# Optimization experiments

Measured on AMD Instinct MI355X. Metric: run time of the kernel, lower is better.

The kernel has to match this reference:

```python
import jax, jax.numpy as jnp
import numpy as np


def setup_inputs() -> dict:
    key = jax.random.key(0)
    ks = jax.random.split(key, 7)
    C = 256
    Cqk = C // 8  # 32
    B, D, H, W = 4, 16, 16, 16
    s_in = 1.0 / np.sqrt(C)  # conv1x1 fan_in = C
    return {
        "x": jax.random.normal(ks[0], (B, C, D, H, W), dtype=jnp.float32),
        "Wq": jax.random.uniform(ks[1], (Cqk, C), jnp.float32, -s_in, s_in),
        "bq": jax.random.uniform(ks[2], (Cqk,), jnp.float32, -s_in, s_in),
        "Wk": jax.random.uniform(ks[3], (Cqk, C), jnp.float32, -s_in, s_in),
        "bk": jax.random.uniform(ks[4], (Cqk,), jnp.float32, -s_in, s_in),
        "Wv": jax.random.uniform(ks[5], (C, C), jnp.float32, -s_in, s_in),
        "bv": jax.random.uniform(ks[6], (C,), jnp.float32, -s_in, s_in),
    }


def reference(x, Wq, bq, Wk, bk, Wv, bv):
    B, C, D, H, W = x.shape
    N = D * H * W
    xf = x.reshape(B, C, N)  # [B, C, N]
    # 1x1x1 convs == per-voxel GEMMs over the channel dim
    q = jnp.einsum('oc,bcn->bon', Wq, xf) + bq[None, :, None]  # [B, Cqk, N]
    k = jnp.einsum('oc,bcn->bon', Wk, xf) + bk[None, :, None]  # [B, Cqk, N]
    v = jnp.einsum('oc,bcn->bon', Wv, xf) + bv[None, :, None]  # [B, C, N]
    # attention[b, n, m] = softmax_m( q[:, n] . k[:, m] )
    scores = jnp.einsum('bcn,bcm->bnm', q, k)  # [B, N, N]
    attn = jax.nn.softmax(scores, axis=-1)
    # out = value @ attention^T  -> out[b, c, n] = sum_m v[b,c,m] * attn[b,n,m]
    out = jnp.einsum('bcm,bnm->bcn', v, attn)
    return x + out.reshape(B, C, D, H, W)
```

## Files before the change

kernel.cpp:

```cpp
#include <hip/hip_runtime.h>
#include <math.h>

#define B_   4
#define C_   256
#define CQK  32
#define N_   4096
#define TQ   32
#define TM   64

typedef __attribute__((ext_vector_type(8))) short short8;
typedef __attribute__((ext_vector_type(4))) short short4v;
typedef __attribute__((ext_vector_type(4))) float f32x4;
typedef __attribute__((ext_vector_type(2))) unsigned int uint2v;

__device__ __forceinline__ unsigned short f2bf(float f) {
    unsigned u = __builtin_bit_cast(unsigned, f);
    u += 0x7fffu + ((u >> 16) & 1u);
    return (unsigned short)(u >> 16);
}

__global__ __launch_bounds__(256) void cvt_w(
    const float* __restrict__ Wq, const float* __restrict__ bq,
    const float* __restrict__ Wk, const float* __restrict__ bk,
    const float* __restrict__ Wv, const float* __restrict__ bv,
    unsigned short* __restrict__ wbf, float* __restrict__ biasf)
{
    const int r = blockIdx.x;
    const int t = threadIdx.x;
    const float* src = (r < 32) ? (Wq + r * C_)
                     : (r < 64) ? (Wk + (r - 32) * C_)
                                : (Wv + (r - 64) * C_);
    wbf[r * C_ + t] = f2bf(src[t]);
    if (t == 0)
        biasf[r] = (r < 32) ? bq[r] : (r < 64) ? bk[r - 32] : bv[r - 64];
}

__global__ __launch_bounds__(256) void proj_qkv(
    const float* __restrict__ x, const unsigned short* __restrict__ wbf,
    const float* __restrict__ biasf,
    unsigned short* __restrict__ qb, unsigned short* __restrict__ kb,
    unsigned short* __restrict__ vb)
{
    __shared__ __align__(16) unsigned short xs[64 * 136];

    const int t    = threadIdx.x;
    const int w    = t >> 6;
    const int lane = t & 63;
    const int quad = lane >> 4;
    const int c16  = lane & 15;
    const int n0   = blockIdx.x * 64;
    const int b    = blockIdx.y;

    f32x4 acc[5][4];
#pragma unroll
    for (int i = 0; i < 5; ++i)
#pragma unroll
        for (int nt = 0; nt < 4; ++nt) acc[i][nt] = (f32x4){0.f, 0.f, 0.f, 0.f};

#pragma unroll
    for (int half = 0; half < 2; ++half) {
        __syncthreads();
#pragma unroll
        for (int pass = 0; pass < 8; ++pass) {
            const int c  = 128 * half + pass * 16 + (t >> 4);
            const int nq = (t & 15) * 4;
            const f32x4 xv = *(const f32x4*)&x[((size_t)(b * C_) + c) * N_ + n0 + nq];
            const int cl = c - 128 * half;
            xs[(nq + 0) * 136 + cl] = f2bf(xv.x);
            xs[(nq + 1) * 136 + cl] = f2bf(xv.y);
            xs[(nq + 2) * 136 + cl] = f2bf(xv.z);
            xs[(nq + 3) * 136 + cl] = f2bf(xv.w);
        }
        __syncthreads();
#pragma unroll
        for (int ks = 0; ks < 4; ++ks) {
            short8 af[5], bf[4];
#pragma unroll
            for (int i = 0; i < 5; ++i) {
                const int o = (5 * w + i) * 16 + c16;
                af[i] = *(const short8*)&wbf[o * C_ + half * 128 + ks * 32 + quad * 8];
            }
#pragma unroll
            for (int nt = 0; nt < 4; ++nt)
                bf[nt] = *(const short8*)&xs[(16 * nt + c16) * 136 + ks * 32 + quad * 8];
#pragma unroll
            for (int i = 0; i < 5; ++i)
#pragma unroll
                for (int nt = 0; nt < 4; ++nt)
                    acc[i][nt] = __builtin_amdgcn_mfma_f32_16x16x32_bf16(af[i], bf[nt], acc[i][nt], 0, 0, 0);
        }
    }

#pragma unroll
    for (int i = 0; i < 5; ++i) {
        const int OT = 5 * w + i;
        const int obase = OT * 16 + 4 * quad;
        const f32x4 bv4 = *(const f32x4*)&biasf[obase];
#pragma unroll
        for (int nt = 0; nt < 4; ++nt) {
            const int n = n0 + 16 * nt + c16;
            float vals[4];
#pragma unroll
            for (int r = 0; r < 4; ++r) vals[r] = acc[i][nt][r] + bv4[r];
            if (OT < 4) {
                unsigned short* dst = (OT < 2) ? qb : kb;
                const int o = obase - ((OT < 2) ? 0 : 32);
                short4v pk;
#pragma unroll
                for (int r = 0; r < 4; ++r) pk[r] = (short)f2bf(vals[r]);
                *(short4v*)&dst[((size_t)(b * N_) + n) * 32 + o] = pk;
            } else {
#pragma unroll
                for (int r = 0; r < 4; ++r) {
                    const int c = obase + r - 64;
                    vb[((size_t)(b * C_) + c) * N_ + n] = f2bf(vals[r]);
                }
            }
        }
    }
}

__global__ __launch_bounds__(256) void attn_kernel(
    const float* __restrict__ x,
    const unsigned short* __restrict__ qg,
    const unsigned short* __restrict__ kg,
    const unsigned short* __restrict__ vg,
    float* __restrict__ out)
{
    __shared__ __align__(16) unsigned short qs[TQ * 40];
    __shared__ __align__(16) unsigned short ks[TM * 40];
    __shared__ __align__(16) unsigned short vs[256 * 64];
    __shared__ __align__(16) unsigned short ps[TQ * 72];
    __shared__ float ls[2 * TQ];

    const int t    = threadIdx.x;
    const int w    = t >> 6;
    const int lane = t & 63;
    const int quad = lane >> 4;
    const int c16  = lane & 15;
    const int b    = blockIdx.y;
    const int q0   = blockIdx.x * TQ;
    const int qh   = w & 1;
    const int kh   = w >> 1;

    if (t < 128) {
        const int row = t >> 2, seg = t & 3;
        *(short8*)&qs[row * 40 + seg * 8] =
            *(const short8*)(qg + ((size_t)(b * N_) + q0 + row) * 32 + seg * 8);
    }

    short8 kpre, vpre[8];
    {
        const int row = t >> 2, seg = t & 3;
        kpre = *(const short8*)(kg + ((size_t)(b * N_) + row) * 32 + seg * 8);
        const int vc = t >> 3, vch = t & 7;
#pragma unroll
        for (int p = 0; p < 8; ++p)
            vpre[p] = *(const short8*)(vg + ((size_t)(b * C_) + vc + 32 * p) * N_ + vch * 8);
    }

    f32x4 O[4][2];
#pragma unroll
    for (int ct = 0; ct < 4; ++ct)
#pragma unroll
        for (int qt = 0; qt < 2; ++qt) O[ct][qt] = (f32x4){0.f, 0.f, 0.f, 0.f};

    float l_run = 0.0f;

#pragma unroll 1
    for (int it = 0; it < N_ / TM; ++it) {
        __syncthreads();
        {
            const int row = t >> 2, seg = t & 3;
            *(short8*)&ks[row * 40 + seg * 8] = kpre;
            const int vc0 = t >> 3, vch = t & 7;
#pragma unroll
            for (int p = 0; p < 8; ++p) {
                const int c = vc0 + 32 * p;
                *(short8*)&vs[c * 64 + 8 * (vch ^ (c & 7))] = vpre[p];
            }
        }
        __syncthreads();
        if (it < N_ / TM - 1) {
            const int m1 = (it + 1) * TM;
            const int row = t >> 2, seg = t & 3;
            kpre = *(const short8*)(kg + ((size_t)(b * N_) + m1 + row) * 32 + seg * 8);
            const int vc = t >> 3, vch = t & 7;
#pragma unroll
            for (int p = 0; p < 8; ++p)
                vpre[p] = *(const short8*)(vg + ((size_t)(b * C_) + vc + 32 * p) * N_ + m1 + vch * 8);
        }

        const short8 bqf = *(const short8*)&qs[(16 * qh + c16) * 40 + quad * 8];
        float rs = 0.f;
#pragma unroll
        for (int f = 0; f < 2; ++f) {
            const short8 akf = *(const short8*)&ks[(32 * kh + 16 * f + c16) * 40 + quad * 8];
            const f32x4 z = {0.f, 0.f, 0.f, 0.f};
            const f32x4 sf = __builtin_amdgcn_mfma_f32_16x16x32_bf16(akf, bqf, z, 0, 0, 0);
            float p4[4];
#pragma unroll
            for (int r = 0; r < 4; ++r) { p4[r] = __expf(sf[r]); rs += p4[r]; }
            uint2v u;
            u.x = (unsigned)f2bf(p4[0]) | ((unsigned)f2bf(p4[1]) << 16);
            u.y = (unsigned)f2bf(p4[2]) | ((unsigned)f2bf(p4[3]) << 16);
            *(uint2v*)&ps[(16 * qh + c16) * 72 + 32 * kh + 16 * f + 4 * quad] = u;
        }
        rs += __shfl_xor(rs, 16);
        rs += __shfl_xor(rs, 32);
        l_run += rs;
        __syncthreads();

#pragma unroll
        for (int s = 0; s < 2; ++s) {
            const short8 bp0 = *(const short8*)&ps[(c16) * 72 + 32 * s + 8 * quad];
            const short8 bp1 = *(const short8*)&ps[(16 + c16) * 72 + 32 * s + 8 * quad];
#pragma unroll
            for (int ct = 0; ct < 4; ++ct) {
                const int c = 64 * w + 16 * ct + c16;
                const short8 av = *(const short8*)&vs[c * 64 + 8 * ((4 * s + quad) ^ (c & 7))];
                O[ct][0] = __builtin_amdgcn_mfma_f32_16x16x32_bf16(av, bp0, O[ct][0], 0, 0, 0);
                O[ct][1] = __builtin_amdgcn_mfma_f32_16x16x32_bf16(av, bp1, O[ct][1], 0, 0, 0);
            }
        }
    }

    if (quad == 0) ls[kh * TQ + 16 * qh + c16] = l_run;
    __syncthreads();

#pragma unroll
    for (int qt = 0; qt < 2; ++qt) {
        const int q = 16 * qt + c16;
        const float li = 1.0f / (ls[q] + ls[TQ + q]);
        const int n = q0 + q;
#pragma unroll
        for (int ct = 0; ct < 4; ++ct) {
#pragma unroll
            for (int r = 0; r < 4; ++r) {
                const int c = 64 * w + 16 * ct + 4 * quad + r;
                const size_t idx = ((size_t)(b * C_) + c) * N_ + n;
                out[idx] = x[idx] + O[ct][qt][r] * li;
            }
        }
    }
}

extern "C" void kernel_launch(void* const* d_in, const int* in_sizes, int n_in,
                              void* d_out, int out_size, void* d_ws, size_t ws_size,
                              hipStream_t stream) {
    const float* x  = (const float*)d_in[0];
    const float* Wq = (const float*)d_in[1];
    const float* bq = (const float*)d_in[2];
    const float* Wk = (const float*)d_in[3];
    const float* bk = (const float*)d_in[4];
    const float* Wv = (const float*)d_in[5];
    const float* bv = (const float*)d_in[6];
    float* out = (float*)d_out;

    unsigned short* ws16 = (unsigned short*)d_ws;
    unsigned short* qb  = ws16;
    unsigned short* kb  = qb + (size_t)B_ * N_ * 32;
    unsigned short* vb  = kb + (size_t)B_ * N_ * 32;
    unsigned short* wbf = vb + (size_t)B_ * C_ * N_;
    float* biasf = (float*)(wbf + 320 * C_);

    cvt_w<<<dim3(320), 256, 0, stream>>>(Wq, bq, Wk, bk, Wv, bv, wbf, biasf);
    proj_qkv<<<dim3(N_ / 64, B_), 256, 0, stream>>>(x, wbf, biasf, qb, kb, vb);
    attn_kernel<<<dim3(N_ / TQ, B_), 256, 0, stream>>>(x, qb, kb, vb, out);
}
```

Baseline: 176.9 us.

## Add bf16 transpose pass, drop LDS staging of K/V, widen attention tile

A new kernel transposes x into a bf16 [N,C] buffer so the projection kernel reads MFMA operands straight from global memory without LDS staging, using smaller 32-voxel tiles. The attention kernel moves to 512 threads and 64 queries per block. It reads K and V fragments directly from global/L2 instead of staging them in shared memory, and double-buffers the P tile so each iteration needs one barrier instead of three. The trade-offs are an extra global pass over x and heavier reliance on cache for V reuse, since V is re-read per wave rather than shared through LDS.

Result: slower. 244.6 us (+38.3%).

```diff
diff --git a/kernel.cpp b/kernel.cpp
--- a/kernel.cpp
+++ b/kernel.cpp
@@ -5,8 +5,10 @@
 #define C_   256
 #define CQK  32
 #define N_   4096
-#define TQ   32
+#define TQ   64
 #define TM   64
+#define ITERS (N_ / TM)
+#define PSS  72
 
 typedef __attribute__((ext_vector_type(8))) short short8;
 typedef __attribute__((ext_vector_type(4))) short short4v;
@@ -35,60 +37,65 @@
         biasf[r] = (r < 32) ? bq[r] : (r < 64) ? bk[r - 32] : bv[r - 64];
 }
 
+__global__ __launch_bounds__(256) void xpose(
+    const float* __restrict__ x, unsigned short* __restrict__ xT)
+{
+    const int n0 = blockIdx.x * 64;
+    const int b  = blockIdx.y;
+    const int nl = threadIdx.x & 63;
+    const int co = (threadIdx.x >> 6) * 8;
+
+    const float* xb = x + (size_t)(b * C_) * N_ + n0 + nl;
+    unsigned short* ob = xT + ((size_t)(b * N_) + n0 + nl) * C_;
+
+#pragma unroll
+    for (int pass = 0; pass < 8; ++pass) {
+        const int c0 = pass * 32 + co;
+        short8 pk;
+#pragma unroll
+        for (int j = 0; j < 8; ++j)
+            pk[j] = (short)f2bf(xb[(size_t)(c0 + j) * N_]);
+        *(short8*)(ob + c0) = pk;
+    }
+}
+
 __global__ __launch_bounds__(256) void proj_qkv(
-    const float* __restrict__ x, const unsigned short* __restrict__ wbf,
+    const unsigned short* __restrict__ xT, const unsigned short* __restrict__ wbf,
     const float* __restrict__ biasf,
     unsigned short* __restrict__ qb, unsigned short* __restrict__ kb,
     unsigned short* __restrict__ vb)
 {
-    __shared__ __align__(16) unsigned short xs[64 * 136];
-
     const int t    = threadIdx.x;
     const int w    = t >> 6;
     const int lane = t & 63;
     const int quad = lane >> 4;
     const int c16  = lane & 15;
-    const int n0   = blockIdx.x * 64;
+    const int n0   = blockIdx.x * 32;
     const int b    = blockIdx.y;
 
-    f32x4 acc[5][4];
+    f32x4 acc[5][2];
 #pragma unroll
     for (int i = 0; i < 5; ++i)
 #pragma unroll
-        for (int nt = 0; nt < 4; ++nt) acc[i][nt] = (f32x4){0.f, 0.f, 0.f, 0.f};
-
-#pragma unroll
-    for (int half = 0; half < 2; ++half) {
-        __syncthreads();
-#pragma unroll
-        for (int pass = 0; pass < 8; ++pass) {
-            const int c  = 128 * half + pass * 16 + (t >> 4);
-            const int nq = (t & 15) * 4;
-            const f32x4 xv = *(const f32x4*)&x[((size_t)(b * C_) + c) * N_ + n0 + nq];
-            const int cl = c - 128 * half;
-            xs[(nq + 0) * 136 + cl] = f2bf(xv.x);
-            xs[(nq + 1) * 136 + cl] = f2bf(xv.y);
-            xs[(nq + 2) * 136 + cl] = f2bf(xv.z);
-            xs[(nq + 3) * 136 + cl] = f2bf(xv.w);
-        }
-        __syncthreads();
-#pragma unroll
-        for (int ks = 0; ks < 4; ++ks) {
-            short8 af[5], bf[4];
-#pragma unroll
-            for (int i = 0; i < 5; ++i) {
-                const int o = (5 * w + i) * 16 + c16;
-                af[i] = *(const short8*)&wbf[o * C_ + half * 128 + ks * 32 + quad * 8];
-            }
-#pragma unroll
-            for (int nt = 0; nt < 4; ++nt)
-                bf[nt] = *(const short8*)&xs[(16 * nt + c16) * 136 + ks * 32 + quad * 8];
-#pragma unroll
-            for (int i = 0; i < 5; ++i)
-#pragma unroll
-                for (int nt = 0; nt < 4; ++nt)
-                    acc[i][nt] = __builtin_amdgcn_mfma_f32_16x16x32_bf16(af[i], bf[nt], acc[i][nt], 0, 0, 0);
-        }
+        for (int nt = 0; nt < 2; ++nt) acc[i][nt] = (f32x4){0.f, 0.f, 0.f, 0.f};
+
+    const unsigned short* xrow0 = xT + ((size_t)(b * N_) + n0 + c16) * C_ + quad * 8;
+    const unsigned short* wrow0 = wbf + (size_t)(80 * w + c16) * C_ + quad * 8;
+
+#pragma unroll
+    for (int ks = 0; ks < 8; ++ks) {
+        short8 af[5], bf[2];
+#pragma unroll
+        for (int i = 0; i < 5; ++i)
+            af[i] = *(const short8*)(wrow0 + (size_t)(16 * i) * C_ + 32 * ks);
+#pragma unroll
+        for (int nt = 0; nt < 2; ++nt)
+            bf[nt] = *(const short8*)(xrow0 + (size_t)(16 * nt) * C_ + 32 * ks);
+#pragma unroll
+        for (int i = 0; i < 5; ++i)
+#pragma unroll
+            for (int nt = 0; nt < 2; ++nt)
+                acc[i][nt] = __builtin_amdgcn_mfma_f32_16x16x32_bf16(af[i], bf[nt], acc[i][nt], 0, 0, 0);
     }
 
 #pragma unroll
@@ -97,7 +104,7 @@
         const int obase = OT * 16 + 4 * quad;
         const f32x4 bv4 = *(const f32x4*)&biasf[obase];
 #pragma unroll
-        for (int nt = 0; nt < 4; ++nt) {
+        for (int nt = 0; nt < 2; ++nt) {
             const int n = n0 + 16 * nt + c16;
             float vals[4];
 #pragma unroll
@@ -120,18 +127,15 @@
     }
 }
 
-__global__ __launch_bounds__(256) void attn_kernel(
+__global__ __launch_bounds__(512) void attn_kernel(
     const float* __restrict__ x,
     const unsigned short* __restrict__ qg,
     const unsigned short* __restrict__ kg,
     const unsigned short* __restrict__ vg,
     float* __restrict__ out)
 {
-    __shared__ __align__(16) unsigned short qs[TQ * 40];
-    __shared__ __align__(16) unsigned short ks[TM * 40];
-    __shared__ __align__(16) unsigned short vs[256 * 64];
-    __shared__ __align__(16) unsigned short ps[TQ * 72];
-    __shared__ float ls[2 * TQ];
+    __shared__ __align__(16) unsigned short ps[2][TQ * PSS];
+    __shared__ float ls[4 * TQ];
 
     const int t    = threadIdx.x;
     const int w    = t >> 6;
@@ -140,24 +144,15 @@
     const int c16  = lane & 15;
     const int b    = blockIdx.y;
     const int q0   = blockIdx.x * TQ;
-    const int qh   = w & 1;
-    const int kh   = w >> 1;
-
-    if (t < 128) {
-        const int row = t >> 2, seg = t & 3;
-        *(short8*)&qs[row * 40 + seg * 8] =
-            *(const short8*)(qg + ((size_t)(b * N_) + q0 + row) * 32 + seg * 8);
-    }
-
-    short8 kpre, vpre[8];
-    {
-        const int row = t >> 2, seg = t & 3;
-        kpre = *(const short8*)(kg + ((size_t)(b * N_) + row) * 32 + seg * 8);
-        const int vc = t >> 3, vch = t & 7;
-#pragma unroll
-        for (int p = 0; p < 8; ++p)
-            vpre[p] = *(const short8*)(vg + ((size_t)(b * C_) + vc + 32 * p) * N_ + vch * 8);
-    }
+    const int fs = w & 3, gp = w >> 2;
+    const int cg = w & 3, qh = w >> 2;
+
+    const unsigned short* kbase = kg + (size_t)(b * N_) * 32;
+    const unsigned short* vbase = vg + (size_t)(b * C_) * N_;
+
+    short8 bq0 = *(const short8*)(qg + ((size_t)(b * N_) + q0 + 16 * (2 * gp) + c16) * 32 + quad * 8);
+    short8 bq1 = *(const short8*)(qg + ((size_t)(b * N_) + q0 + 16 * (2 * gp + 1) + c16) * 32 + quad * 8);
+    short8 ak = *(const short8*)(kbase + (size_t)(fs * 16 + c16) * 32 + quad * 8);
 
     f32x4 O[4][2];
 #pragma unroll
@@ -165,79 +160,75 @@
 #pragma unroll
         for (int qt = 0; qt < 2; ++qt) O[ct][qt] = (f32x4){0.f, 0.f, 0.f, 0.f};
 
-    float l_run = 0.0f;
+    float l0 = 0.f, l1 = 0.f;
+    int buf = 0;
 
 #pragma unroll 1
-    for (int it = 0; it < N_ / TM; ++it) {
+    for (int it = 0; it < ITERS; ++it) {
+        const f32x4 z = {0.f, 0.f, 0.f, 0.f};
+        const f32x4 s0 = __builtin_amdgcn_mfma_f32_16x16x32_bf16(ak, bq0, z, 0, 0, 0);
+        const f32x4 s1 = __builtin_amdgcn_mfma_f32_16x16x32_bf16(ak, bq1, z, 0, 0, 0);
+        if (it < ITERS - 1)
+            ak = *(const short8*)(kbase + (size_t)((it + 1) * TM + fs * 16 + c16) * 32 + quad * 8);
+
+        float p0[4], p1[4];
+        float rs0 = 0.f, rs1 = 0.f;
+#pragma unroll
+        for (int r = 0; r < 4; ++r) {
+            p0[r] = __expf(s0[r]); rs0 += p0[r];
+            p1[r] = __expf(s1[r]); rs1 += p1[r];
+        }
+        rs0 += __shfl_xor(rs0, 16); rs0 += __shfl_xor(rs0, 32);
+        rs1 += __shfl_xor(rs1, 16); rs1 += __shfl_xor(rs1, 32);
+        l0 += rs0; l1 += rs1;
+
+        uint2v u0, u1;
+        u0.x = (unsigned)f2bf(p0[0]) | ((unsigned)f2bf(p0[1]) << 16);
+        u0.y = (unsigned)f2bf(p0[2]) | ((unsigned)f2bf(p0[3]) << 16);
+        u1.x = (unsigned)f2bf(p1[0]) | ((unsigned)f2bf(p1[1]) << 16);
+        u1.y = (unsigned)f2bf(p1[2]) | ((unsigned)f2bf(p1[3]) << 16);
+        const int kvc = fs * 16 + 4 * quad;
+        *(uint2v*)&ps[buf][(16 * (2 * gp) + c16) * PSS + kvc]     = u0;
+        *(uint2v*)&ps[buf][(16 * (2 * gp + 1) + c16) * PSS + kvc] = u1;
+
         __syncthreads();
-        {
-            const int row = t >> 2, seg = t & 3;
-            *(short8*)&ks[row * 40 + seg * 8] = kpre;
-            const int vc0 = t >> 3, vch = t & 7;
-#pragma unroll
-            for (int p = 0; p < 8; ++p) {
-                const int c = vc0 + 32 * p;
-                *(short8*)&vs[c * 64 + 8 * (vch ^ (c & 7))] = vpre[p];
+
+        const int kv0 = it * TM;
+        short8 bp[2][2];
+#pragma unroll
+        for (int qt = 0; qt < 2; ++qt)
+#pragma unroll
+            for (int s = 0; s < 2; ++s)
+                bp[qt][s] = *(const short8*)&ps[buf][(32 * qh + 16 * qt + c16) * PSS + 32 * s + 8 * quad];
+
+#pragma unroll
+        for (int s = 0; s < 2; ++s)
+#pragma unroll
+            for (int ct = 0; ct < 4; ++ct) {
+                const short8 av = *(const short8*)(
+                    vbase + (size_t)(64 * cg + 16 * ct + c16) * N_ + kv0 + 32 * s + 8 * quad);
+                O[ct][0] = __builtin_amdgcn_mfma_f32_16x16x32_bf16(av, bp[0][s], O[ct][0], 0, 0, 0);
+                O[ct][1] = __builtin_amdgcn_mfma_f32_16x16x32_bf16(av, bp[1][s], O[ct][1], 0, 0, 0);
             }
-        }
-        __syncthreads();
-        if (it < N_ / TM - 1) {
-            const int m1 = (it + 1) * TM;
-            const int row = t >> 2, seg = t & 3;
-            kpre = *(const short8*)(kg + ((size_t)(b * N_) + m1 + row) * 32 + seg * 8);
-            const int vc = t >> 3, vch = t & 7;
-#pragma unroll
-            for (int p = 0; p < 8; ++p)
-                vpre[p] = *(const short8*)(vg + ((size_t)(b * C_) + vc + 32 * p) * N_ + m1 + vch * 8);
-        }
-
-        const short8 bqf = *(const short8*)&qs[(16 * qh + c16) * 40 + quad * 8];
-        float rs = 0.f;
-#pragma unroll
-        for (int f = 0; f < 2; ++f) {
-            const short8 akf = *(const short8*)&ks[(32 * kh + 16 * f + c16) * 40 + quad * 8];
-            const f32x4 z = {0.f, 0.f, 0.f, 0.f};
-            const f32x4 sf = __builtin_amdgcn_mfma_f32_16x16x32_bf16(akf, bqf, z, 0, 0, 0);
-            float p4[4];
-#pragma unroll
-            for (int r = 0; r < 4; ++r) { p4[r] = __expf(sf[r]); rs += p4[r]; }
-            uint2v u;
-            u.x = (unsigned)f2bf(p4[0]) | ((unsigned)f2bf(p4[1]) << 16);
-            u.y = (unsigned)f2bf(p4[2]) | ((unsigned)f2bf(p4[3]) << 16);
-            *(uint2v*)&ps[(16 * qh + c16) * 72 + 32 * kh + 16 * f + 4 * quad] = u;
-        }
-        rs += __shfl_xor(rs, 16);
-        rs += __shfl_xor(rs, 32);
-        l_run += rs;
-        __syncthreads();
-
-#pragma unroll
-        for (int s = 0; s < 2; ++s) {
-            const short8 bp0 = *(const short8*)&ps[(c16) * 72 + 32 * s + 8 * quad];
-            const short8 bp1 = *(const short8*)&ps[(16 + c16) * 72 + 32 * s + 8 * quad];
-#pragma unroll
-            for (int ct = 0; ct < 4; ++ct) {
-                const int c = 64 * w + 16 * ct + c16;
-                const short8 av = *(const short8*)&vs[c * 64 + 8 * ((4 * s + quad) ^ (c & 7))];
-                O[ct][0] = __builtin_amdgcn_mfma_f32_16x16x32_bf16(av, bp0, O[ct][0], 0, 0, 0);
-                O[ct][1] = __builtin_amdgcn_mfma_f32_16x16x32_bf16(av, bp1, O[ct][1], 0, 0, 0);
-            }
-        }
-    }
-
-    if (quad == 0) ls[kh * TQ + 16 * qh + c16] = l_run;
+        buf ^= 1;
+    }
+
+    if (quad == 0) {
+        ls[fs * TQ + 16 * (2 * gp) + c16]     = l0;
+        ls[fs * TQ + 16 * (2 * gp + 1) + c16] = l1;
+    }
     __syncthreads();
 
 #pragma unroll
     for (int qt = 0; qt < 2; ++qt) {
-        const int q = 16 * qt + c16;
-        const float li = 1.0f / (ls[q] + ls[TQ + q]);
+        const int q = 32 * qh + 16 * qt + c16;
+        const float li = 1.0f / (ls[q] + ls[TQ + q] + ls[2 * TQ + q] + ls[3 * TQ + q]);
         const int n = q0 + q;
 #pragma unroll
         for (int ct = 0; ct < 4; ++ct) {
 #pragma unroll
             for (int r = 0; r < 4; ++r) {
-                const int c = 64 * w + 16 * ct + 4 * quad + r;
+                const int c = 64 * cg + 16 * ct + 4 * quad + r;
                 const size_t idx = ((size_t)(b * C_) + c) * N_ + n;
                 out[idx] = x[idx] + O[ct][qt][r] * li;
             }
@@ -261,10 +252,12 @@
     unsigned short* qb  = ws16;
     unsigned short* kb  = qb + (size_t)B_ * N_ * 32;
     unsigned short* vb  = kb + (size_t)B_ * N_ * 32;
-    unsigned short* wbf = vb + (size_t)B_ * C_ * N_;
+    unsigned short* xT  = vb + (size_t)B_ * C_ * N_;
+    unsigned short* wbf = xT + (size_t)B_ * N_ * C_;
     float* biasf = (float*)(wbf + 320 * C_);
 
     cvt_w<<<dim3(320), 256, 0, stream>>>(Wq, bq, Wk, bk, Wv, bv, wbf, biasf);
-    proj_qkv<<<dim3(N_ / 64, B_), 256, 0, stream>>>(x, wbf, biasf, qb, kb, vb);
-    attn_kernel<<<dim3(N_ / TQ, B_), 256, 0, stream>>>(x, qb, kb, vb, out);
-}
+    xpose<<<dim3(N_ / 64, B_), 256, 0, stream>>>(x, xT);
+    proj_qkv<<<dim3(N_ / 32, B_), 256, 0, stream>>>(xT, wbf, biasf, qb, kb, vb);
+    attn_kernel<<<dim3(N_ / TQ, B_), 512, 0, stream>>>(x, qb, kb, vb, out);
+}
```
